# Optimization experiments

Hardware: AMD Instinct MI355X
Metric: run time of the kernel (lower is better)

## Reference

```python
import jax, jax.numpy as jnp
import numpy as np

B, T, C = 8, 1024, 1024
H, D = 16, 64  # num_heads, head_size

def setup_inputs() -> dict:
    key = jax.random.key(0)
    ks = jax.random.split(key, 6)
    s = C ** -0.5
    return {
        "x": jax.random.normal(ks[0], (B, T, C), dtype=jnp.float32),
        "Wq": jax.random.normal(ks[1], (H, C, D), dtype=jnp.float32) * s,
        "Wk": jax.random.normal(ks[2], (H, C, D), dtype=jnp.float32) * s,
        "Wv": jax.random.normal(ks[3], (H, C, D), dtype=jnp.float32) * s,
        "Wproj": jax.random.normal(ks[4], (H * D, C), dtype=jnp.float32) * ((H * D) ** -0.5),
        "bproj": jnp.zeros((C,), dtype=jnp.float32),
    }

def reference(x, Wq, Wk, Wv, Wproj, bproj):
    # per-head QKV projections, batched over heads via einsum (same math as looped heads)
    q = jnp.einsum('btc,hcd->bhtd', x, Wq)
    k = jnp.einsum('btc,hcd->bhtd', x, Wk)
    v = jnp.einsum('btc,hcd->bhtd', x, Wv)
    scale = D ** -0.5  # k.shape[-1]**-0.5 in original head
    scores = jnp.einsum('bhtd,bhsd->bhts', q, k) * scale  # [B,H,T,T]
    Tn = x.shape[1]
    causal = jnp.tril(jnp.ones((Tn, Tn), dtype=bool))
    scores = jnp.where(causal, scores, jnp.float32(-jnp.inf))
    att = jax.nn.softmax(scores, axis=-1)
    out = jnp.einsum('bhts,bhsd->bhtd', att, v)          # [B,H,T,D]
    out = out.transpose(0, 2, 1, 3).reshape(x.shape[0], Tn, H * D)  # concat heads
    return out @ Wproj + bproj  # dropout is identity at p=0.0
```

## Files before the change

### kernel.cpp

```cpp
#include <hip/hip_runtime.h>
#include <hip/hip_bf16.h>

#define B_ 8
#define T_ 1024
#define C_ 1024
#define H_ 16
#define D_ 64
#define QKVLD 3072

typedef short v4s __attribute__((ext_vector_type(4)));
typedef short v8s __attribute__((ext_vector_type(8)));
typedef float v4f __attribute__((ext_vector_type(4)));
typedef float v16f __attribute__((ext_vector_type(16)));

__device__ __forceinline__ unsigned short f2b(float f) {
    unsigned int u = __builtin_bit_cast(unsigned int, f);
    unsigned int lsb = (u >> 16) & 1u;
    u += 0x7fffu + lsb;
    return (unsigned short)(u >> 16);
}

__device__ __forceinline__ float fexp2(float x) {
    return __expf(x * 0.69314718056f);
}

__device__ __forceinline__ v4s pack4(float p0, float p1, float p2, float p3) {
    unsigned int a = (__builtin_bit_cast(unsigned int, p0) + 0x8000u) >> 16;
    unsigned int b = (__builtin_bit_cast(unsigned int, p1) + 0x8000u) & 0xFFFF0000u;
    unsigned int c = (__builtin_bit_cast(unsigned int, p2) + 0x8000u) >> 16;
    unsigned int d = (__builtin_bit_cast(unsigned int, p3) + 0x8000u) & 0xFFFF0000u;
    union { unsigned int u[2]; v4s v; } t;
    t.u[0] = a | b; t.u[1] = c | d;
    return t.v;
}

#define MFMA32(A, B, C) __builtin_amdgcn_mfma_f32_16x16x32_bf16(A, B, C, 0, 0, 0)
#define MFMA16(A, B, C) __builtin_amdgcn_mfma_f32_16x16x16bf16_1k(A, B, C, 0, 0, 0)

#define GLOAD16(gp, lp)                                                          \
    __builtin_amdgcn_global_load_lds(                                            \
        (const __attribute__((address_space(1))) unsigned int*)(gp),             \
        (__attribute__((address_space(3))) unsigned int*)(lp), 16, 0, 0)

__global__ void prep_kernel(const float* __restrict__ x, const float* __restrict__ Wq,
                            const float* __restrict__ Wk, const float* __restrict__ Wv,
                            const float* __restrict__ Wproj,
                            unsigned short* __restrict__ xb,
                            unsigned short* __restrict__ WqkvT,
                            unsigned short* __restrict__ WprojT) {
    __shared__ unsigned short t[64][65];
    int g = blockIdx.x;
    if (g < 8192) {
        int i = (g * 256 + (int)threadIdx.x) * 4;
        float4 v = *(const float4*)(x + i);
        ushort4 o;
        o.x = f2b(v.x); o.y = f2b(v.y); o.z = f2b(v.z); o.w = f2b(v.w);
        *(ushort4*)(xb + i) = o;
    } else if (g < 8192 + 768) {
        int idx = g - 8192;
        int z = idx >> 4;
        int h = z / 3, part = z % 3;
        const float* src = (part == 0 ? Wq : (part == 1 ? Wk : Wv)) + (size_t)h * C_ * D_;
        int c0 = (idx & 15) * 64;
        for (int i = threadIdx.x; i < 4096; i += 256) {
            int r = i >> 6, d = i & 63;
            t[d][r] = f2b(src[(size_t)(c0 + r) * D_ + d]);
        }
        __syncthreads();
        unsigned short* dst = WqkvT + (size_t)(part * 1024 + h * 64) * C_;
        for (int i = threadIdx.x; i < 4096; i += 256) {
            int d = i >> 6, r = i & 63;
            dst[(size_t)d * C_ + c0 + r] = t[d][r];
        }
    } else {
        int idx = g - 8960;
        int n0 = (idx & 15) * 64, k0 = (idx >> 4) * 64;
        for (int i = threadIdx.x; i < 4096; i += 256) {
            int r = i >> 6, c = i & 63;
            t[c][r] = f2b(Wproj[(size_t)(k0 + r) * C_ + n0 + c]);
        }
        __syncthreads();
        for (int i = threadIdx.x; i < 4096; i += 256) {
            int n = i >> 6, k = i & 63;
            WprojT[(size_t)(n0 + n) * 1024 + k0 + k] = t[n][k];
        }
    }
}

__global__ __launch_bounds__(256, 2) void gemm_qk(const unsigned short* __restrict__ A,
                                                  const unsigned short* __restrict__ Bt,
                                                  unsigned short* __restrict__ Cout,
                                                  int M, int N, int K, int ldc) {
    constexpr int ABUF = 256 * 32;
    constexpr int BBUF = 128 * 32;
    __shared__ unsigned short smem[2 * ABUF + 2 * BBUF];
    unsigned short* lA0 = smem;
    unsigned short* lB0 = smem + 2 * ABUF;

    int tid = threadIdx.x;
    int m0 = blockIdx.y * 256, n0 = blockIdx.x * 128;
    int lane = tid & 63, w = tid >> 6;
    int half = lane >> 5, l32 = lane & 31;
    int wm = w >> 1, wn = w & 1;

    const unsigned short* gA[4];
    int offA[4];
    #pragma unroll
    for (int j = 0; j < 4; j++) {
        int c = j * 256 + tid;
        int row = c >> 2;
        int col8 = ((c & 3) ^ ((row >> 1) & 3)) * 8;
        gA[j] = A + (size_t)(m0 + row) * K + col8;
        offA[j] = (j * 256 + w * 64) * 16;
    }
    const unsigned short* gB[2];
    int offB[2];
    #pragma unroll
    for (int j = 0; j < 2; j++) {
        int c = j * 256 + tid;
        int row = c >> 2;
        int col8 = ((c & 3) ^ ((row >> 1) & 3)) * 8;
        gB[j] = Bt + (size_t)(n0 + row) * K + col8;
        offB[j] = (j * 256 + w * 64) * 16;
    }

    int am[4], bn[2];
    #pragma unroll
    for (int mi = 0; mi < 4; mi++) am[mi] = wm * 128 + mi * 32 + l32;
    #pragma unroll
    for (int ni = 0; ni < 2; ni++) bn[ni] = wn * 64 + ni * 32 + l32;

    v16f acc[4][2];
    #pragma unroll
    for (int mi = 0; mi < 4; mi++)
        #pragma unroll
        for (int ni = 0; ni < 2; ni++)
            #pragma unroll
            for (int r = 0; r < 16; r++) acc[mi][ni][r] = 0.f;

    int ktiles = K >> 5;
    #pragma unroll
    for (int j = 0; j < 4; j++) GLOAD16(gA[j], (char*)lA0 + offA[j]);
    #pragma unroll
    for (int j = 0; j < 2; j++) GLOAD16(gB[j], (char*)lB0 + offB[j]);

    for (int it = 0; it < ktiles; it++) {
        int cur = it & 1, nxt = cur ^ 1;
        __asm__ volatile("s_waitcnt vmcnt(0)" ::: "memory");
        __asm__ volatile("s_barrier" ::: "memory");
        {
            int kn = (it + 1 < ktiles) ? (it + 1) * 32 : it * 32;
            #pragma unroll
            for (int j = 0; j < 4; j++) GLOAD16(gA[j] + kn, (char*)(lA0 + nxt * ABUF) + offA[j]);
            #pragma unroll
            for (int j = 0; j < 2; j++) GLOAD16(gB[j] + kn, (char*)(lB0 + nxt * BBUF) + offB[j]);
        }
        const unsigned short* bufA = lA0 + cur * ABUF;
        const unsigned short* bufB = lB0 + cur * BBUF;
        #pragma unroll
        for (int step = 0; step < 2; step++) {
            int g = step * 2 + half;
            v8s af[4], bf[2];
            #pragma unroll
            for (int mi = 0; mi < 4; mi++)
                af[mi] = *(const v8s*)&bufA[am[mi] * 32 + ((g ^ ((am[mi] >> 1) & 3)) * 8)];
            #pragma unroll
            for (int ni = 0; ni < 2; ni++)
                bf[ni] = *(const v8s*)&bufB[bn[ni] * 32 + ((g ^ ((bn[ni] >> 1) & 3)) * 8)];
            #pragma unroll
            for (int mi = 0; mi < 4; mi++)
                #pragma unroll
                for (int ni = 0; ni < 2; ni++)
                    acc[mi][ni] = __builtin_amdgcn_mfma_f32_32x32x16_bf16(af[mi], bf[ni], acc[mi][ni], 0, 0, 0);
        }
    }
    #pragma unroll
    for (int mi = 0; mi < 4; mi++) {
        #pragma unroll
        for (int ni = 0; ni < 2; ni++) {
            int col = n0 + wn * 64 + ni * 32 + l32;
            #pragma unroll
            for (int r = 0; r < 16; r++) {
                int row = m0 + wm * 128 + mi * 32 + (r & 3) + 8 * (r >> 2) + 4 * half;
                Cout[(size_t)row * ldc + col] = f2b(acc[mi][ni][r]);
            }
        }
    }
}

__global__ __launch_bounds__(256, 3) void gemm_v(const unsigned short* __restrict__ A,
                                                 const unsigned short* __restrict__ Bt,
                                                 unsigned short* __restrict__ Vt,
                                                 int M, int N, int K) {
    constexpr int ABUF = 128 * 32;
    constexpr int BBUF = 128 * 32;
    __shared__ unsigned short lA[3 * ABUF];
    __shared__ unsigned short lB[3 * BBUF];

    int tid = threadIdx.x;
    int lane = tid & 63, w = tid >> 6;
    int half = lane >> 5, l32 = lane & 31;
    int wm = w >> 1, wn = w & 1;

    int g = blockIdx.x;
    int nbm = M / 128;
    int stripe = nbm >> 3;
    int xcd = g & 7, s = g >> 3;
    int m0 = (xcd * stripe + (s % stripe)) * 128;
    int n0 = (s / stripe) * 128;

    const unsigned short* gA[2];
    int offA[2];
    #pragma unroll
    for (int j = 0; j < 2; j++) {
        int c = j * 256 + tid;
        int row = c >> 2;
        int col8 = ((c & 3) ^ ((row >> 1) & 3)) * 8;
        gA[j] = A + (size_t)(m0 + row) * K + col8;
        offA[j] = (j * 256 + w * 64) * 16;
    }
    const unsigned short* gB[2];
    int offB[2];
    #pragma unroll
    for (int j = 0; j < 2; j++) {
        int c = j * 256 + tid;
        int row = c >> 2;
        int col8 = ((c & 3) ^ ((row >> 1) & 3)) * 8;
        gB[j] = Bt + (size_t)(n0 + row) * K + col8;
        offB[j] = (j * 256 + w * 64) * 16;
    }

    int am[2], bn[2];
    #pragma unroll
    for (int mi = 0; mi < 2; mi++) am[mi] = wm * 64 + mi * 32 + l32;
    #pragma unroll
    for (int ni = 0; ni < 2; ni++) bn[ni] = wn * 64 + ni * 32 + l32;

    v16f acc[2][2];
    #pragma unroll
    for (int mi = 0; mi < 2; mi++)
        #pragma unroll
        for (int ni = 0; ni < 2; ni++)
            #pragma unroll
            for (int r = 0; r < 16; r++) acc[mi][ni][r] = 0.f;

    int kt = K >> 5;
    #pragma unroll
    for (int j = 0; j < 2; j++) GLOAD16(gA[j], (char*)lA + offA[j]);
    #pragma unroll
    for (int j = 0; j < 2; j++) GLOAD16(gB[j], (char*)lB + offB[j]);
    #pragma unroll
    for (int j = 0; j < 2; j++) GLOAD16(gA[j] + 32, (char*)(lA + ABUF) + offA[j]);
    #pragma unroll
    for (int j = 0; j < 2; j++) GLOAD16(gB[j] + 32, (char*)(lB + BBUF) + offB[j]);

    int cur = 0;
    for (int it = 0; it < kt; it++) {
        int nx2 = cur + 2; if (nx2 >= 3) nx2 -= 3;
        __asm__ volatile("s_waitcnt vmcnt(4)" ::: "memory");
        __asm__ volatile("s_barrier" ::: "memory");
        {
            int kn = ((it + 2 < kt) ? it + 2 : kt - 1) << 5;
            #pragma unroll
            for (int j = 0; j < 2; j++) GLOAD16(gA[j] + kn, (char*)(lA + nx2 * ABUF) + offA[j]);
            #pragma unroll
            for (int j = 0; j < 2; j++) GLOAD16(gB[j] + kn, (char*)(lB + nx2 * BBUF) + offB[j]);
        }
        const unsigned short* bufA = lA + cur * ABUF;
        const unsigned short* bufB = lB + cur * BBUF;
        #pragma unroll
        for (int step = 0; step < 2; step++) {
            int gch = step * 2 + half;
            v8s af[2], bf[2];
            #pragma unroll
            for (int mi = 0; mi < 2; mi++)
                af[mi] = *(const v8s*)&bufA[am[mi] * 32 + ((gch ^ ((am[mi] >> 1) & 3)) * 8)];
            #pragma unroll
            for (int ni = 0; ni < 2; ni++)
                bf[ni] = *(const v8s*)&bufB[bn[ni] * 32 + ((gch ^ ((bn[ni] >> 1) & 3)) * 8)];
            #pragma unroll
            for (int mi = 0; mi < 2; mi++)
                #pragma unroll
                for (int ni = 0; ni < 2; ni++)
                    acc[mi][ni] = __builtin_amdgcn_mfma_f32_32x32x16_bf16(af[mi], bf[ni], acc[mi][ni], 0, 0, 0);
        }
        cur = cur + 1; if (cur >= 3) cur -= 3;
    }
    unsigned short* sT = lA;
    int bB = m0 >> 10;
    int t0 = m0 & 1023;
    #pragma unroll
    for (int p = 0; p < 2; p++) {
        __syncthreads();
        if (wn == p) {
            #pragma unroll
            for (int mi = 0; mi < 2; mi++)
                #pragma unroll
                for (int ni = 0; ni < 2; ni++) {
                    int cl = ni * 32 + l32;
                    #pragma unroll
                    for (int r = 0; r < 16; r++) {
                        int rowl = wm * 64 + mi * 32 + (r & 3) + 8 * (r >> 2) + 4 * half;
                        sT[cl * 136 + rowl] = f2b(acc[mi][ni][r]);
                    }
                }
        }
        __syncthreads();
        #pragma unroll
        for (int j = 0; j < 4; j++) {
            int c = j * 256 + tid;
            int cl = c >> 4, ch = c & 15;
            int vcol = n0 + p * 64 + cl;
            int hh = vcol >> 6, dd = vcol & 63;
            *(v8s*)&Vt[(((size_t)bB * 16 + hh) * 64 + dd) * T_ + t0 + ch * 8] =
                *(const v8s*)&sT[cl * 136 + ch * 8];
        }
    }
}

__global__ __launch_bounds__(256, 3) void gemm_proj(const unsigned short* __restrict__ A,
                                                    const unsigned short* __restrict__ Bt,
                                                    float* __restrict__ Cout,
                                                    const float* __restrict__ bias,
                                                    int M, int N, int K) {
    constexpr int ABUF = 128 * 32;
    constexpr int BBUF = 128 * 32;
    __shared__ unsigned short lA[3 * ABUF];
    __shared__ unsigned short lB[3 * BBUF];

    int tid = threadIdx.x;
    int lane = tid & 63, w = tid >> 6;
    int half = lane >> 5, l32 = lane & 31;
    int wm = w >> 1, wn = w & 1;

    int g = blockIdx.x;
    int nbm = M / 128;
    int stripe = nbm >> 3;
    int xcd = g & 7, s = g >> 3;
    int m0 = (xcd * stripe + (s % stripe)) * 128;
    int n0 = (s / stripe) * 128;

    const unsigned short* gA[2];
    int offA[2];
    #pragma unroll
    for (int j = 0; j < 2; j++) {
        int c = j * 256 + tid;
        int row = c >> 2;
        int col8 = ((c & 3) ^ ((row >> 1) & 3)) * 8;
        gA[j] = A + (size_t)(m0 + row) * K + col8;
        offA[j] = (j * 256 + w * 64) * 16;
    }
    const unsigned short* gB[2];
    int offB[2];
    #pragma unroll
    for (int j = 0; j < 2; j++) {
        int c = j * 256 + tid;
        int row = c >> 2;
        int col8 = ((c & 3) ^ ((row >> 1) & 3)) * 8;
        gB[j] = Bt + (size_t)(n0 + row) * K + col8;
        offB[j] = (j * 256 + w * 64) * 16;
    }

    int am[2], bn[2];
    #pragma unroll
    for (int mi = 0; mi < 2; mi++) am[mi] = wm * 64 + mi * 32 + l32;
    #pragma unroll
    for (int ni = 0; ni < 2; ni++) bn[ni] = wn * 64 + ni * 32 + l32;

    v16f acc[2][2];
    #pragma unroll
    for (int mi = 0; mi < 2; mi++)
        #pragma unroll
        for (int ni = 0; ni < 2; ni++)
            #pragma unroll
            for (int r = 0; r < 16; r++) acc[mi][ni][r] = 0.f;

    int kt = K >> 5;
    #pragma unroll
    for (int j = 0; j < 2; j++) GLOAD16(gA[j], (char*)lA + offA[j]);
    #pragma unroll
    for (int j = 0; j < 2; j++) GLOAD16(gB[j], (char*)lB + offB[j]);
    #pragma unroll
    for (int j = 0; j < 2; j++) GLOAD16(gA[j] + 32, (char*)(lA + ABUF) + offA[j]);
    #pragma unroll
    for (int j = 0; j < 2; j++) GLOAD16(gB[j] + 32, (char*)(lB + BBUF) + offB[j]);

    int cur = 0;
    for (int it = 0; it < kt; it++) {
        int nx2 = cur + 2; if (nx2 >= 3) nx2 -= 3;
        __asm__ volatile("s_waitcnt vmcnt(4)" ::: "memory");
        __asm__ volatile("s_barrier" ::: "memory");
        {
            int kn = ((it + 2 < kt) ? it + 2 : kt - 1) << 5;
            #pragma unroll
            for (int j = 0; j < 2; j++) GLOAD16(gA[j] + kn, (char*)(lA + nx2 * ABUF) + offA[j]);
            #pragma unroll
            for (int j = 0; j < 2; j++) GLOAD16(gB[j] + kn, (char*)(lB + nx2 * BBUF) + offB[j]);
        }
        const unsigned short* bufA = lA + cur * ABUF;
        const unsigned short* bufB = lB + cur * BBUF;
        #pragma unroll
        for (int step = 0; step < 2; step++) {
            int gch = step * 2 + half;
            v8s af[2], bf[2];
            #pragma unroll
            for (int mi = 0; mi < 2; mi++)
                af[mi] = *(const v8s*)&bufA[am[mi] * 32 + ((gch ^ ((am[mi] >> 1) & 3)) * 8)];
            #pragma unroll
            for (int ni = 0; ni < 2; ni++)
                bf[ni] = *(const v8s*)&bufB[bn[ni] * 32 + ((gch ^ ((bn[ni] >> 1) & 3)) * 8)];
            #pragma unroll
            for (int mi = 0; mi < 2; mi++)
                #pragma unroll
                for (int ni = 0; ni < 2; ni++)
                    acc[mi][ni] = __builtin_amdgcn_mfma_f32_32x32x16_bf16(af[mi], bf[ni], acc[mi][ni], 0, 0, 0);
        }
        cur = cur + 1; if (cur >= 3) cur -= 3;
    }
    #pragma unroll
    for (int mi = 0; mi < 2; mi++) {
        #pragma unroll
        for (int ni = 0; ni < 2; ni++) {
            int col = n0 + wn * 64 + ni * 32 + l32;
            #pragma unroll
            for (int r = 0; r < 16; r++) {
                int row = m0 + wm * 64 + mi * 32 + (r & 3) + 8 * (r >> 2) + 4 * half;
                Cout[(size_t)row * N + col] = acc[mi][ni][r] + bias[col];
            }
        }
    }
}

__global__ __launch_bounds__(256) void attn_kernel(const unsigned short* __restrict__ QKV,
                                                   const unsigned short* __restrict__ Vt,
                                                   unsigned short* __restrict__ Ob) {
    int bh = blockIdx.x;
    int qt = 7 - blockIdx.y;
    int b = bh >> 4, h = bh & 15;
    int tid = threadIdx.x, lane = tid & 63, w = tid >> 6;
    int quad = lane >> 4, l16 = lane & 15;
    int qg0 = qt * 128 + w * 32;

    __shared__ unsigned short lK[2][2][64][32];
    __shared__ unsigned short lV[2][64][32];

    v8s aq[2][2];
    #pragma unroll
    for (int st = 0; st < 2; st++) {
        const unsigned short* qp = QKV + (size_t)(b * T_ + qg0 + st * 16 + l16) * QKVLD + h * 64;
        aq[st][0] = *(const v8s*)(qp + quad * 8);
        aq[st][1] = *(const v8s*)(qp + 32 + quad * 8);
    }

    const unsigned short* gK[2];
    const unsigned short* gV[2];
    int ldsOff[2];
    #pragma unroll
    for (int j = 0; j < 2; j++) {
        int c = j * 256 + tid;
        int halfp = c >> 8, row = (c >> 2) & 63;
        int col8 = ((c & 3) ^ ((row >> 1) & 3)) * 8;
        gK[j] = QKV + (size_t)(b * T_ + row) * QKVLD + 1024 + h * 64 + halfp * 32 + col8;
        gV[j] = Vt + ((size_t)bh * 64 + row) * T_ + halfp * 32 + col8;
        ldsOff[j] = (j * 256 + w * 64) * 16;
    }
    int rcol = (quad ^ ((l16 >> 1) & 3)) * 8;

    v4f accO[2][4];
    float lsum[2] = {0.f, 0.f};
    #pragma unroll
    for (int st = 0; st < 2; st++)
        #pragma unroll
        for (int i = 0; i < 4; i++) accO[st][i] = (v4f){0.f, 0.f, 0.f, 0.f};

    int ntiles = 2 * qt + 2;
    const float SC = 0.1803368801f;

    #pragma unroll
    for (int j = 0; j < 2; j++)
        GLOAD16(gK[j], (char*)&lK[0][0][0][0] + ldsOff[j]);

    for (int it = 0; it < ntiles; it++) {
        int cur = it & 1, nxt = cur ^ 1;
        int s0 = it * 64;
        __asm__ volatile("s_waitcnt vmcnt(0)" ::: "memory");
        __asm__ volatile("s_barrier" ::: "memory");
        #pragma unroll
        for (int j = 0; j < 2; j++)
            GLOAD16(gV[j] + s0, (char*)&lV[0][0][0] + ldsOff[j]);
        __asm__ volatile("" ::: "memory");
        {
            int itn = (it + 1 < ntiles) ? it + 1 : it;
            size_t koff = (size_t)itn * 64 * QKVLD;
            #pragma unroll
            for (int j = 0; j < 2; j++)
                GLOAD16(gK[j] + koff, (char*)&lK[nxt][0][0][0] + ldsOff[j]);
        }
        bool act0 = (qg0 + 15 >= s0);
        bool act1 = (qg0 + 31 >= s0);
        v4s pP[2][4];
        if (act1) {
            v4f sf[2][4];
            #pragma unroll
            for (int nt = 0; nt < 4; nt++) {
                v8s bk0 = *(const v8s*)&lK[cur][0][nt * 16 + l16][rcol];
                v8s bk1 = *(const v8s*)&lK[cur][1][nt * 16 + l16][rcol];
                v4f a1 = (v4f){0.f, 0.f, 0.f, 0.f};
                a1 = MFMA32(bk0, aq[1][0], a1);
                a1 = MFMA32(bk1, aq[1][1], a1);
                sf[1][nt] = a1;
                if (act0) {
                    v4f a0 = (v4f){0.f, 0.f, 0.f, 0.f};
                    a0 = MFMA32(bk0, aq[0][0], a0);
                    a0 = MFMA32(bk1, aq[0][1], a0);
                    sf[0][nt] = a0;
                }
            }
            bool diag = (it >= ntiles - 2);
            #pragma unroll
            for (int st = 0; st < 2; st++) {
                if (st == 0 && !act0) continue;
                int qg = qg0 + st * 16 + l16;
                #pragma unroll
                for (int nt = 0; nt < 4; nt++) {
                    float p[4];
                    #pragma unroll
                    for (int r = 0; r < 4; r++) {
                        if (diag) {
                            int sg = s0 + nt * 16 + quad * 4 + r;
                            p[r] = (sg > qg) ? 0.f : fexp2(sf[st][nt][r] * SC);
                        } else {
                            p[r] = fexp2(sf[st][nt][r] * SC);
                        }
                        lsum[st] += p[r];
                    }
                    pP[st][nt] = pack4(p[0], p[1], p[2], p[3]);
                }
            }
        }
        __asm__ volatile("s_waitcnt vmcnt(2)" ::: "memory");
        __asm__ volatile("s_barrier" ::: "memory");
        if (act1) {
            #pragma unroll
            for (int kb = 0; kb < 4; kb++) {
                int sc_ = kb >> 1;
                int ccg = (kb & 1) * 2 + (quad >> 1);
                #pragma unroll
                for (int dt = 0; dt < 4; dt++) {
                    int d = dt * 16 + l16;
                    int ccp = ccg ^ ((l16 >> 1) & 3);
                    v4s bv = *(const v4s*)&lV[sc_][d][ccp * 8 + (quad & 1) * 4];
                    accO[1][dt] = MFMA16(pP[1][kb], bv, accO[1][dt]);
                    if (act0) accO[0][dt] = MFMA16(pP[0][kb], bv, accO[0][dt]);
                }
            }
        }
    }
    #pragma unroll
    for (int st = 0; st < 2; st++) {
        float ls = lsum[st];
        ls += __shfl_xor(ls, 16, 64);
        ls += __shfl_xor(ls, 32, 64);
        #pragma unroll
        for (int r = 0; r < 4; r++) {
            float lq = __shfl(ls, quad * 4 + r, 64);
            float inv = 1.0f / lq;
            int q = qg0 + st * 16 + quad * 4 + r;
            #pragma unroll
            for (int dt = 0; dt < 4; dt++) {
                int d = dt * 16 + l16;
                Ob[(size_t)(b * T_ + q) * (H_ * D_) + h * 64 + d] = f2b(accO[st][dt][r] * inv);
            }
        }
    }
}

extern "C" void kernel_launch(void* const* d_in, const int* in_sizes, int n_in,
                              void* d_out, int out_size, void* d_ws, size_t ws_size,
                              hipStream_t stream) {
    const float* x     = (const float*)d_in[0];
    const float* Wq    = (const float*)d_in[1];
    const float* Wk    = (const float*)d_in[2];
    const float* Wv    = (const float*)d_in[3];
    const float* Wproj = (const float*)d_in[4];
    const float* bproj = (const float*)d_in[5];
    float* out = (float*)d_out;

    char* ws = (char*)d_ws;
    unsigned short* xb     = (unsigned short*)ws;
    unsigned short* WqkvT  = (unsigned short*)(ws + 16777216);
    unsigned short* WprojT = (unsigned short*)(ws + 23068672);
    unsigned short* QKV    = (unsigned short*)(ws + 25165824);
    unsigned short* Vt     = (unsigned short*)(ws + 75497472);
    unsigned short* Ob     = (unsigned short*)(ws + 92274688);

    prep_kernel<<<dim3(9216), dim3(256), 0, stream>>>(x, Wq, Wk, Wv, Wproj, xb, WqkvT, WprojT);
    gemm_qk<<<dim3(16, 32), dim3(256), 0, stream>>>(xb, WqkvT, QKV, 8192, 2048, 1024, QKVLD);
    gemm_v<<<dim3(512), dim3(256), 0, stream>>>(xb, WqkvT + (size_t)2048 * 1024, Vt, 8192, 1024, 1024);
    attn_kernel<<<dim3(128, 8), dim3(256), 0, stream>>>(QKV, Vt, Ob);
    gemm_proj<<<dim3(512), dim3(256), 0, stream>>>(Ob, WprojT, out, bproj, 8192, 1024, 1024);
}
```

Before: 244.4 us.

## Shrink attention query tiles to 64 rows and fold softmax scale into K

The attention kernel now gives each block 64 query rows, one 16-row strip per wave, instead of 128. That doubles the grid and removes the idle-strip predication. V is now double-buffered alongside K, so the mid-loop wait and barrier are gone. The 1/sqrt(D) scale is folded into K at the QK GEMM epilogue, so the exp runs directly on the scores. The cost is more K/V reloads per query, since each key tile now serves fewer queries.

After: 235.7 us. 1.04x faster.

```diff
diff --git a/kernel.cpp b/kernel.cpp
--- a/kernel.cpp
+++ b/kernel.cpp
@@ -18,10 +18,6 @@
     unsigned int lsb = (u >> 16) & 1u;
     u += 0x7fffu + lsb;
     return (unsigned short)(u >> 16);
-}
-
-__device__ __forceinline__ float fexp2(float x) {
-    return __expf(x * 0.69314718056f);
 }
 
 __device__ __forceinline__ v4s pack4(float p0, float p1, float p2, float p3) {
@@ -174,6 +170,7 @@
                     acc[mi][ni] = __builtin_amdgcn_mfma_f32_32x32x16_bf16(af[mi], bf[ni], acc[mi][ni], 0, 0, 0);
         }
     }
+    float scl = (n0 >= 1024) ? 0.125f : 1.0f;
     #pragma unroll
     for (int mi = 0; mi < 4; mi++) {
         #pragma unroll
@@ -182,7 +179,7 @@
             #pragma unroll
             for (int r = 0; r < 16; r++) {
                 int row = m0 + wm * 128 + mi * 32 + (r & 3) + 8 * (r >> 2) + 4 * half;
-                Cout[(size_t)row * ldc + col] = f2b(acc[mi][ni][r]);
+                Cout[(size_t)row * ldc + col] = f2b(acc[mi][ni][r] * scl);
             }
         }
     }
@@ -435,21 +432,20 @@
                                                    const unsigned short* __restrict__ Vt,
                                                    unsigned short* __restrict__ Ob) {
     int bh = blockIdx.x;
-    int qt = 7 - blockIdx.y;
+    int qt = 15 - blockIdx.y;
     int b = bh >> 4, h = bh & 15;
     int tid = threadIdx.x, lane = tid & 63, w = tid >> 6;
     int quad = lane >> 4, l16 = lane & 15;
-    int qg0 = qt * 128 + w * 32;
+    int qg0 = qt * 64 + w * 16;
 
     __shared__ unsigned short lK[2][2][64][32];
-    __shared__ unsigned short lV[2][64][32];
-
-    v8s aq[2][2];
-    #pragma unroll
-    for (int st = 0; st < 2; st++) {
-        const unsigned short* qp = QKV + (size_t)(b * T_ + qg0 + st * 16 + l16) * QKVLD + h * 64;
-        aq[st][0] = *(const v8s*)(qp + quad * 8);
-        aq[st][1] = *(const v8s*)(qp + 32 + quad * 8);
+    __shared__ unsigned short lV[2][2][64][32];
+
+    v8s aq0, aq1;
+    {
+        const unsigned short* qp = QKV + (size_t)(b * T_ + qg0 + l16) * QKVLD + h * 64;
+        aq0 = *(const v8s*)(qp + quad * 8);
+        aq1 = *(const v8s*)(qp + 32 + quad * 8);
     }
 
     const unsigned short* gK[2];
@@ -466,111 +462,87 @@
     }
     int rcol = (quad ^ ((l16 >> 1) & 3)) * 8;
 
-    v4f accO[2][4];
-    float lsum[2] = {0.f, 0.f};
-    #pragma unroll
-    for (int st = 0; st < 2; st++)
-        #pragma unroll
-        for (int i = 0; i < 4; i++) accO[st][i] = (v4f){0.f, 0.f, 0.f, 0.f};
-
-    int ntiles = 2 * qt + 2;
-    const float SC = 0.1803368801f;
-
-    #pragma unroll
-    for (int j = 0; j < 2; j++)
-        GLOAD16(gK[j], (char*)&lK[0][0][0][0] + ldsOff[j]);
+    v4f accO[4];
+    float lsum = 0.f;
+    #pragma unroll
+    for (int i = 0; i < 4; i++) accO[i] = (v4f){0.f, 0.f, 0.f, 0.f};
+
+    int ntiles = qt + 1;
+
+    #pragma unroll
+    for (int j = 0; j < 2; j++) GLOAD16(gK[j], (char*)&lK[0][0][0][0] + ldsOff[j]);
+    #pragma unroll
+    for (int j = 0; j < 2; j++) GLOAD16(gV[j], (char*)&lV[0][0][0][0] + ldsOff[j]);
 
     for (int it = 0; it < ntiles; it++) {
         int cur = it & 1, nxt = cur ^ 1;
         int s0 = it * 64;
         __asm__ volatile("s_waitcnt vmcnt(0)" ::: "memory");
         __asm__ volatile("s_barrier" ::: "memory");
-        #pragma unroll
-        for (int j = 0; j < 2; j++)
-            GLOAD16(gV[j] + s0, (char*)&lV[0][0][0] + ldsOff[j]);
-        __asm__ volatile("" ::: "memory");
         {
             int itn = (it + 1 < ntiles) ? it + 1 : it;
             size_t koff = (size_t)itn * 64 * QKVLD;
             #pragma unroll
             for (int j = 0; j < 2; j++)
                 GLOAD16(gK[j] + koff, (char*)&lK[nxt][0][0][0] + ldsOff[j]);
-        }
-        bool act0 = (qg0 + 15 >= s0);
-        bool act1 = (qg0 + 31 >= s0);
-        v4s pP[2][4];
-        if (act1) {
-            v4f sf[2][4];
-            #pragma unroll
-            for (int nt = 0; nt < 4; nt++) {
-                v8s bk0 = *(const v8s*)&lK[cur][0][nt * 16 + l16][rcol];
-                v8s bk1 = *(const v8s*)&lK[cur][1][nt * 16 + l16][rcol];
-                v4f a1 = (v4f){0.f, 0.f, 0.f, 0.f};
-                a1 = MFMA32(bk0, aq[1][0], a1);
-                a1 = MFMA32(bk1, aq[1][1], a1);
-                sf[1][nt] = a1;
-                if (act0) {
-                    v4f a0 = (v4f){0.f, 0.f, 0.f, 0.f};
-                    a0 = MFMA32(bk0, aq[0][0], a0);
-                    a0 = MFMA32(bk1, aq[0][1], a0);
-                    sf[0][nt] = a0;
+            size_t voff = (size_t)itn * 64;
+            #pragma unroll
+            for (int j = 0; j < 2; j++)
+                GLOAD16(gV[j] + voff, (char*)&lV[nxt][0][0][0] + ldsOff[j]);
+        }
+        v4f sf[4];
+        #pragma unroll
+        for (int nt = 0; nt < 4; nt++) {
+            v8s bk0 = *(const v8s*)&lK[cur][0][nt * 16 + l16][rcol];
+            v8s bk1 = *(const v8s*)&lK[cur][1][nt * 16 + l16][rcol];
+            v4f a = (v4f){0.f, 0.f, 0.f, 0.f};
+            a = MFMA32(bk0, aq0, a);
+            a = MFMA32(bk1, aq1, a);
+            sf[nt] = a;
+        }
+        bool diag = (it == ntiles - 1);
+        int qg = qg0 + l16;
+        v4s pP[4];
+        #pragma unroll
+        for (int nt = 0; nt < 4; nt++) {
+            float p[4];
+            #pragma unroll
+            for (int r = 0; r < 4; r++) {
+                float e = __expf(sf[nt][r]);
+                if (diag) {
+                    int sg = s0 + nt * 16 + quad * 4 + r;
+                    e = (sg > qg) ? 0.f : e;
                 }
+                p[r] = e;
+                lsum += e;
             }
-            bool diag = (it >= ntiles - 2);
-            #pragma unroll
-            for (int st = 0; st < 2; st++) {
-                if (st == 0 && !act0) continue;
-                int qg = qg0 + st * 16 + l16;
-                #pragma unroll
-                for (int nt = 0; nt < 4; nt++) {
-                    float p[4];
-                    #pragma unroll
-                    for (int r = 0; r < 4; r++) {
-                        if (diag) {
-                            int sg = s0 + nt * 16 + quad * 4 + r;
-                            p[r] = (sg > qg) ? 0.f : fexp2(sf[st][nt][r] * SC);
-                        } else {
-                            p[r] = fexp2(sf[st][nt][r] * SC);
-                        }
-                        lsum[st] += p[r];
-                    }
-                    pP[st][nt] = pack4(p[0], p[1], p[2], p[3]);
-                }
-            }
-        }
-        __asm__ volatile("s_waitcnt vmcnt(2)" ::: "memory");
-        __asm__ volatile("s_barrier" ::: "memory");
-        if (act1) {
-            #pragma unroll
-            for (int kb = 0; kb < 4; kb++) {
-                int sc_ = kb >> 1;
-                int ccg = (kb & 1) * 2 + (quad >> 1);
-                #pragma unroll
-                for (int dt = 0; dt < 4; dt++) {
-                    int d = dt * 16 + l16;
-                    int ccp = ccg ^ ((l16 >> 1) & 3);
-                    v4s bv = *(const v4s*)&lV[sc_][d][ccp * 8 + (quad & 1) * 4];
-                    accO[1][dt] = MFMA16(pP[1][kb], bv, accO[1][dt]);
-                    if (act0) accO[0][dt] = MFMA16(pP[0][kb], bv, accO[0][dt]);
-                }
-            }
-        }
-    }
-    #pragma unroll
-    for (int st = 0; st < 2; st++) {
-        float ls = lsum[st];
-        ls += __shfl_xor(ls, 16, 64);
-        ls += __shfl_xor(ls, 32, 64);
-        #pragma unroll
-        for (int r = 0; r < 4; r++) {
-            float lq = __shfl(ls, quad * 4 + r, 64);
-            float inv = 1.0f / lq;
-            int q = qg0 + st * 16 + quad * 4 + r;
+            pP[nt] = pack4(p[0], p[1], p[2], p[3]);
+        }
+        #pragma unroll
+        for (int kb = 0; kb < 4; kb++) {
+            int sc_ = kb >> 1;
+            int ccg = (kb & 1) * 2 + (quad >> 1);
             #pragma unroll
             for (int dt = 0; dt < 4; dt++) {
                 int d = dt * 16 + l16;
-                Ob[(size_t)(b * T_ + q) * (H_ * D_) + h * 64 + d] = f2b(accO[st][dt][r] * inv);
+                int ccp = ccg ^ ((l16 >> 1) & 3);
+                v4s bv = *(const v4s*)&lV[cur][sc_][d][ccp * 8 + (quad & 1) * 4];
+                accO[dt] = MFMA16(pP[kb], bv, accO[dt]);
             }
+        }
+    }
+    float ls = lsum;
+    ls += __shfl_xor(ls, 16, 64);
+    ls += __shfl_xor(ls, 32, 64);
+    #pragma unroll
+    for (int r = 0; r < 4; r++) {
+        float lq = __shfl(ls, quad * 4 + r, 64);
+        float inv = 1.0f / lq;
+        int q = qg0 + quad * 4 + r;
+        #pragma unroll
+        for (int dt = 0; dt < 4; dt++) {
+            int d = dt * 16 + l16;
+            Ob[(size_t)(b * T_ + q) * (H_ * D_) + h * 64 + d] = f2b(accO[dt][r] * inv);
         }
     }
 }
@@ -597,6 +569,6 @@
     prep_kernel<<<dim3(9216), dim3(256), 0, stream>>>(x, Wq, Wk, Wv, Wproj, xb, WqkvT, WprojT);
     gemm_qk<<<dim3(16, 32), dim3(256), 0, stream>>>(xb, WqkvT, QKV, 8192, 2048, 1024, QKVLD);
     gemm_v<<<dim3(512), dim3(256), 0, stream>>>(xb, WqkvT + (size_t)2048 * 1024, Vt, 8192, 1024, 1024);
-    attn_kernel<<<dim3(128, 8), dim3(256), 0, stream>>>(QKV, Vt, Ob);
+    attn_kernel<<<dim3(128, 16), dim3(256), 0, stream>>>(QKV, Vt, Ob);
     gemm_proj<<<dim3(512), dim3(256), 0, stream>>>(Ob, WprojT, out, bproj, 8192, 1024, 1024);
 }
```
